# Kernel optimization log

Hardware: AMD Instinct MI355X
Metric: run time of the kernel (lower is better)

## Reference

```python
import jax, jax.numpy as jnp
import numpy as np

N = 8192
F_IN, F_HID, F_OUT = 256, 256, 64


def setup_inputs() -> dict:
    key = jax.random.key(0)
    k1, k2, k3, k4 = jax.random.split(key, 4)
    adj = jax.random.uniform(k1, (N, N), dtype=jnp.float32)
    x = jax.random.normal(k2, (N, F_IN), dtype=jnp.float32)
    W1 = jax.random.uniform(k3, (F_IN, F_HID), dtype=jnp.float32)
    W2 = jax.random.uniform(k4, (F_HID, F_OUT), dtype=jnp.float32)
    return {"adj": adj, "x": x, "W1": W1, "W2": W2}


def reference(adj, x, W1, W2):
    # Layer 1: left_to_right -> (adj @ x) @ W1, then ReLU (dropout is identity in eval)
    h = jnp.matmul(jnp.matmul(adj, x), W1)
    h = jax.nn.relu(h)
    # Layer 2 (last): no activation
    h = jnp.matmul(jnp.matmul(adj, h), W2)
    # Final log_softmax over class dim
    return jax.nn.log_softmax(h, axis=1)
```

## Files before the change

### kernel.cpp

```cpp
#include <hip/hip_runtime.h>

typedef short bf16x8 __attribute__((ext_vector_type(8)));
typedef float f32x4 __attribute__((ext_vector_type(4)));
typedef unsigned short us8 __attribute__((ext_vector_type(8)));

__device__ __forceinline__ unsigned short f2bf(float f) {
    unsigned int u = __float_as_uint(f);
    u += 0x7fffu + ((u >> 16) & 1u);
    return (unsigned short)(u >> 16);
}

__device__ __forceinline__ void hard_barrier() {
    asm volatile("s_waitcnt lgkmcnt(0)" ::: "memory");
    __builtin_amdgcn_sched_barrier(0);
    __builtin_amdgcn_s_barrier();
    __builtin_amdgcn_sched_barrier(0);
}

__global__ __launch_bounds__(256) void transpose_cast_kernel(
    const float* __restrict__ in, unsigned short* __restrict__ out, int R, int Cc) {
    __shared__ alignas(16) unsigned short sT[64][65];
    const int r0 = blockIdx.x * 64, c0 = blockIdx.y * 64;
    const int t = threadIdx.x;
#pragma unroll
    for (int p = 0; p < 16; ++p) {
        int flat = p * 256 + t;
        int r = flat >> 6, c = flat & 63;
        sT[c][r] = f2bf(in[(size_t)(r0 + r) * Cc + (c0 + c)]);
    }
    __syncthreads();
#pragma unroll
    for (int p = 0; p < 16; ++p) {
        int flat = p * 256 + t;
        int c = flat >> 6, r = flat & 63;
        out[(size_t)(c0 + c) * R + (r0 + r)] = sT[c][r];
    }
}

template<int BN, int WM, int WN, int AMODE, bool TOUT, typename OutT>
__global__ __launch_bounds__(256) void gemm_kernel(
    const void* __restrict__ Aptr, const unsigned short* __restrict__ BT,
    OutT* __restrict__ C, int M, int N, int K, long aslab) {
    constexpr int BM = 64, BK = 64, LDW = 72;
    constexpr int MF = BM / WM / 16;
    constexpr int NF = BN / WN / 16;
    __shared__ alignas(16) unsigned short sA[BM * LDW];
    __shared__ alignas(16) unsigned short sB[BN * LDW];
    const int t = threadIdx.x;
    const int w = t >> 6, l = t & 63;
    const int wr = w / WN, wc = w % WN;
    const int m0 = blockIdx.x * BM;

    f32x4 acc[MF][NF] = {};

    for (int k0 = 0; k0 < K; k0 += BK) {
        const float* A32 = (const float*)Aptr;
#pragma unroll
        for (int p = 0; p < 4; ++p) {
            int flat = p * 256 + t;
            int row = flat >> 4, c4 = flat & 15;
            size_t base = (size_t)(m0 + row) * K + k0 + c4 * 4;
            float4 v = *(const float4*)&A32[base];
            if constexpr (AMODE == 2) {
                float4 b = *(const float4*)&A32[aslab + base];
                float4 c = *(const float4*)&A32[2 * aslab + base];
                float4 d = *(const float4*)&A32[3 * aslab + base];
                v.x = fmaxf(v.x + b.x + c.x + d.x, 0.f);
                v.y = fmaxf(v.y + b.y + c.y + d.y, 0.f);
                v.z = fmaxf(v.z + b.z + c.z + d.z, 0.f);
                v.w = fmaxf(v.w + b.w + c.w + d.w, 0.f);
            }
            ushort4 o = make_ushort4(f2bf(v.x), f2bf(v.y), f2bf(v.z), f2bf(v.w));
            *(ushort4*)&sA[row * LDW + c4 * 4] = o;
        }
#pragma unroll
        for (int p = 0; p < BN * 8 / 256; ++p) {
            int flat = p * 256 + t;
            int row = flat >> 3, c8 = flat & 7;
            us8 v = *(const us8*)&BT[(size_t)row * K + k0 + c8 * 8];
            *(us8*)&sB[row * LDW + c8 * 8] = v;
        }
        __syncthreads();
#pragma unroll
        for (int kk = 0; kk < BK; kk += 32) {
            bf16x8 av[MF], bv[NF];
#pragma unroll
            for (int m = 0; m < MF; ++m)
                av[m] = *(const bf16x8*)&sA[(wr * (BM / WM) + m * 16 + (l & 15)) * LDW + kk + (l >> 4) * 8];
#pragma unroll
            for (int n = 0; n < NF; ++n)
                bv[n] = *(const bf16x8*)&sB[(wc * (BN / WN) + n * 16 + (l & 15)) * LDW + kk + (l >> 4) * 8];
#pragma unroll
            for (int m = 0; m < MF; ++m)
#pragma unroll
                for (int n = 0; n < NF; ++n)
                    acc[m][n] = __builtin_amdgcn_mfma_f32_16x16x32_bf16(av[m], bv[n], acc[m][n], 0, 0, 0);
        }
        __syncthreads();
    }

#pragma unroll
    for (int m = 0; m < MF; ++m) {
#pragma unroll
        for (int n = 0; n < NF; ++n) {
            const int col = wc * (BN / WN) + n * 16 + (l & 15);
            const int rb = m0 + wr * (BM / WM) + m * 16 + ((l >> 4) << 2);
            float v0 = acc[m][n][0], v1 = acc[m][n][1], v2 = acc[m][n][2], v3 = acc[m][n][3];
            if constexpr (TOUT) {
                ushort4 o = make_ushort4(f2bf(v0), f2bf(v1), f2bf(v2), f2bf(v3));
                *(ushort4*)((unsigned short*)C + (size_t)col * M + rb) = o;
            } else {
                C[(size_t)(rb + 0) * N + col] = (OutT)v0;
                C[(size_t)(rb + 1) * N + col] = (OutT)v1;
                C[(size_t)(rb + 2) * N + col] = (OutT)v2;
                C[(size_t)(rb + 3) * N + col] = (OutT)v3;
            }
        }
    }
}

template<int BM, int BN, int WM, int WN, int THREADS, int MINB>
__global__ __launch_bounds__(THREADS, MINB) void pipe_gemm_kernel(
    const float* __restrict__ A, const unsigned short* __restrict__ BT,
    float* __restrict__ C, int M, int N, int K) {
    constexpr int BK = 64, LDW = 72;
    constexpr int MF = BM / WM / 16, NF = BN / WN / 16;
    constexpr int ACH = BM * BK / 4 / THREADS;
    constexpr int BCH = BN * BK / 8 / THREADS;
    static_assert(ACH * THREADS * 4 == BM * BK && BCH * THREADS * 8 == BN * BK, "split");
    __shared__ alignas(16) unsigned short sA[2][BM * LDW];
    __shared__ alignas(16) unsigned short sB[2][BN * LDW];
    const int t = threadIdx.x, w = t >> 6, l = t & 63;
    const int wr = w / WN, wc = w % WN;
    const int nx = gridDim.x;
    const int lin = blockIdx.x + nx * blockIdx.z;
    const int cpx = (nx * gridDim.z) >> 3;
    const int sw = (lin & 7) * cpx + (lin >> 3);
    const int bx = sw % nx, bz = sw / nx;
    const int m0 = bx * BM;
    const int klen = K / gridDim.z, kbeg = bz * klen;
    const int NT = klen / BK;
    float* Cp = C + (size_t)bz * M * N;

    float4 a0[ACH], a1[ACH];
    us8 b0[BCH], b1[BCH];

    auto LOAD = [&](float4 (&ar)[ACH], us8 (&br)[BCH], int k0) {
#pragma unroll
        for (int p = 0; p < ACH; ++p) {
            int flat = p * THREADS + t, row = flat >> 4, c4 = flat & 15;
            ar[p] = *(const float4*)&A[(size_t)(m0 + row) * K + k0 + c4 * 4];
        }
#pragma unroll
        for (int p = 0; p < BCH; ++p) {
            int flat = p * THREADS + t, row = flat >> 3, c8 = flat & 7;
            br[p] = *(const us8*)&BT[(size_t)row * K + k0 + c8 * 8];
        }
    };
    auto WRITE = [&](float4 (&ar)[ACH], us8 (&br)[BCH], int buf) {
#pragma unroll
        for (int p = 0; p < ACH; ++p) {
            int flat = p * THREADS + t, row = flat >> 4, c4 = flat & 15;
            float4 v = ar[p];
            *(ushort4*)&sA[buf][row * LDW + c4 * 4] =
                make_ushort4(f2bf(v.x), f2bf(v.y), f2bf(v.z), f2bf(v.w));
        }
#pragma unroll
        for (int p = 0; p < BCH; ++p) {
            int flat = p * THREADS + t, row = flat >> 3, c8 = flat & 7;
            *(us8*)&sB[buf][row * LDW + c8 * 8] = br[p];
        }
    };

    f32x4 acc[MF][NF] = {};

    auto COMPUTE = [&](int buf) {
#pragma unroll
        for (int kk = 0; kk < BK; kk += 32) {
            bf16x8 av[MF], bv[NF];
#pragma unroll
            for (int m = 0; m < MF; ++m)
                av[m] = *(const bf16x8*)&sA[buf][(wr * (BM / WM) + m * 16 + (l & 15)) * LDW + kk + (l >> 4) * 8];
#pragma unroll
            for (int n = 0; n < NF; ++n)
                bv[n] = *(const bf16x8*)&sB[buf][(wc * (BN / WN) + n * 16 + (l & 15)) * LDW + kk + (l >> 4) * 8];
#pragma unroll
            for (int m = 0; m < MF; ++m)
#pragma unroll
                for (int n = 0; n < NF; ++n)
                    acc[m][n] = __builtin_amdgcn_mfma_f32_16x16x32_bf16(av[m], bv[n], acc[m][n], 0, 0, 0);
        }
    };

    LOAD(a0, b0, kbeg);
    LOAD(a1, b1, kbeg + BK);
    WRITE(a0, b0, 0);
    hard_barrier();

    for (int tt = 0; tt < NT; tt += 2) {
        if (tt + 2 < NT) LOAD(a0, b0, kbeg + (tt + 2) * BK);
        __builtin_amdgcn_sched_barrier(0);
        COMPUTE(0);
        if (tt + 1 < NT) WRITE(a1, b1, 1);
        hard_barrier();
        if (tt + 1 < NT) {
            if (tt + 3 < NT) LOAD(a1, b1, kbeg + (tt + 3) * BK);
            __builtin_amdgcn_sched_barrier(0);
            COMPUTE(1);
            if (tt + 2 < NT) WRITE(a0, b0, 0);
            hard_barrier();
        }
    }

#pragma unroll
    for (int m = 0; m < MF; ++m)
#pragma unroll
        for (int n = 0; n < NF; ++n) {
            const int col = wc * (BN / WN) + n * 16 + (l & 15);
            const int rb = m0 + wr * (BM / WM) + m * 16 + ((l >> 4) << 2);
#pragma unroll
            for (int j = 0; j < 4; ++j)
                Cp[(size_t)(rb + j) * N + col] = acc[m][n][j];
        }
}

__global__ __launch_bounds__(256) void head2_kernel(
    const float* __restrict__ p, float* __restrict__ out, int M) {
    const int t = threadIdx.x, w = t >> 6, l = t & 63;
    const size_t stride = (size_t)M * 64;
#pragma unroll
    for (int rr = 0; rr < 4; ++rr) {
        int i = blockIdx.x * 16 + w * 4 + rr;
        size_t off = (size_t)i * 64 + l;
        float v = 0.f;
#pragma unroll
        for (int s = 0; s < 8; ++s) v += p[s * stride + off];
        float mx = v;
#pragma unroll
        for (int o = 32; o; o >>= 1) mx = fmaxf(mx, __shfl_xor(mx, o));
        float d0 = v - mx;
        float e = __expf(d0);
#pragma unroll
        for (int o = 32; o; o >>= 1) e += __shfl_xor(e, o);
        out[off] = d0 - __logf(e);
    }
}

extern "C" void kernel_launch(void* const* d_in, const int* in_sizes, int n_in,
                              void* d_out, int out_size, void* d_ws, size_t ws_size,
                              hipStream_t stream) {
    const float* adj = (const float*)d_in[0];
    const float* x   = (const float*)d_in[1];
    const float* W1  = (const float*)d_in[2];
    const float* W2  = (const float*)d_in[3];
    float* out = (float*)d_out;

    const int M = 8192, K = 8192;
    char* ws = (char*)d_ws;
    float*          pbuf1 = (float*)ws;
    float*          pbuf2 = (float*)(ws + 33554432);
    unsigned short* zT    = (unsigned short*)(ws + 50331648);
    unsigned short* hwT   = (unsigned short*)(ws + 54525952);
    unsigned short* W1T   = (unsigned short*)(ws + 55574528);
    unsigned short* W2T   = (unsigned short*)(ws + 55705600);

    transpose_cast_kernel<<<dim3(4, 4), 256, 0, stream>>>(W1, W1T, 256, 256);
    transpose_cast_kernel<<<dim3(4, 1), 256, 0, stream>>>(W2, W2T, 256, 64);
    gemm_kernel<256, 1, 4, 1, true, unsigned short>
        <<<dim3(M / 64), 256, 0, stream>>>(x, W1T, zT, M, 256, 256, 0);
    pipe_gemm_kernel<128, 256, 4, 4, 1024, 1>
        <<<dim3(M / 128, 1, 4), 1024, 0, stream>>>(adj, zT, pbuf1, M, 256, K);
    gemm_kernel<64, 2, 2, 2, true, unsigned short>
        <<<dim3(M / 64), 256, 0, stream>>>(pbuf1, W2T, hwT, M, 64, 256, (long)M * 256);
    pipe_gemm_kernel<128, 64, 4, 2, 512, 2>
        <<<dim3(M / 128, 1, 8), 512, 0, stream>>>(adj, hwT, pbuf2, M, 64, K);
    head2_kernel<<<dim3(M / 16), 256, 0, stream>>>(pbuf2, out, M);
}
```

Baseline: 158.0 us.

## Write bf16 copy of adj in first pass and reuse it in second GEMM

The first adjacency GEMM now writes its bf16-converted A tiles out to a workspace buffer as a side effect. The second adjacency GEMM then reads that bf16 copy instead of the fp32 adj, halving its A-operand traffic. The extra 128MB write in the first pass costs bandwidth, so the net gain depends on the second pass being memory-bound. The MFMA inner loop is also reordered to load B fragments one at a time, which lowers register pressure.

New measurement: 179.4 us. 13.5% more time.

```diff
diff --git a/kernel.cpp b/kernel.cpp
--- a/kernel.cpp
+++ b/kernel.cpp
@@ -1,4 +1,5 @@
 #include <hip/hip_runtime.h>
+#include <type_traits>
 
 typedef short bf16x8 __attribute__((ext_vector_type(8)));
 typedef float f32x4 __attribute__((ext_vector_type(4)));
@@ -119,15 +120,15 @@
     }
 }
 
-template<int BM, int BN, int WM, int WN, int THREADS, int MINB>
+template<int BM, int BN, int WM, int WN, int THREADS, int MINB, bool ABF16, bool ASIDE>
 __global__ __launch_bounds__(THREADS, MINB) void pipe_gemm_kernel(
-    const float* __restrict__ A, const unsigned short* __restrict__ BT,
-    float* __restrict__ C, int M, int N, int K) {
+    const void* __restrict__ Aptr, const unsigned short* __restrict__ BT,
+    float* __restrict__ C, unsigned short* __restrict__ Aside, int M, int N, int K) {
     constexpr int BK = 64, LDW = 72;
     constexpr int MF = BM / WM / 16, NF = BN / WN / 16;
-    constexpr int ACH = BM * BK / 4 / THREADS;
+    constexpr int ACH = ABF16 ? (BM * BK / 8 / THREADS) : (BM * BK / 4 / THREADS);
     constexpr int BCH = BN * BK / 8 / THREADS;
-    static_assert(ACH * THREADS * 4 == BM * BK && BCH * THREADS * 8 == BN * BK, "split");
+    using AT = typename std::conditional<ABF16, us8, float4>::type;
     __shared__ alignas(16) unsigned short sA[2][BM * LDW];
     __shared__ alignas(16) unsigned short sB[2][BN * LDW];
     const int t = threadIdx.x, w = t >> 6, l = t & 63;
@@ -142,14 +143,20 @@
     const int NT = klen / BK;
     float* Cp = C + (size_t)bz * M * N;
 
-    float4 a0[ACH], a1[ACH];
+    AT a0[ACH], a1[ACH];
     us8 b0[BCH], b1[BCH];
 
-    auto LOAD = [&](float4 (&ar)[ACH], us8 (&br)[BCH], int k0) {
+    auto LOAD = [&](AT (&ar)[ACH], us8 (&br)[BCH], int k0) {
 #pragma unroll
         for (int p = 0; p < ACH; ++p) {
-            int flat = p * THREADS + t, row = flat >> 4, c4 = flat & 15;
-            ar[p] = *(const float4*)&A[(size_t)(m0 + row) * K + k0 + c4 * 4];
+            int flat = p * THREADS + t;
+            if constexpr (ABF16) {
+                int row = flat >> 3, c8 = flat & 7;
+                ar[p] = *(const us8*)&((const unsigned short*)Aptr)[(size_t)(m0 + row) * K + k0 + c8 * 8];
+            } else {
+                int row = flat >> 4, c4 = flat & 15;
+                ar[p] = *(const float4*)&((const float*)Aptr)[(size_t)(m0 + row) * K + k0 + c4 * 4];
+            }
         }
 #pragma unroll
         for (int p = 0; p < BCH; ++p) {
@@ -157,13 +164,21 @@
             br[p] = *(const us8*)&BT[(size_t)row * K + k0 + c8 * 8];
         }
     };
-    auto WRITE = [&](float4 (&ar)[ACH], us8 (&br)[BCH], int buf) {
+    auto WRITE = [&](AT (&ar)[ACH], us8 (&br)[BCH], int buf, int k0) {
 #pragma unroll
         for (int p = 0; p < ACH; ++p) {
-            int flat = p * THREADS + t, row = flat >> 4, c4 = flat & 15;
-            float4 v = ar[p];
-            *(ushort4*)&sA[buf][row * LDW + c4 * 4] =
-                make_ushort4(f2bf(v.x), f2bf(v.y), f2bf(v.z), f2bf(v.w));
+            int flat = p * THREADS + t;
+            if constexpr (ABF16) {
+                int row = flat >> 3, c8 = flat & 7;
+                *(us8*)&sA[buf][row * LDW + c8 * 8] = ar[p];
+            } else {
+                int row = flat >> 4, c4 = flat & 15;
+                float4 v = ar[p];
+                ushort4 o = make_ushort4(f2bf(v.x), f2bf(v.y), f2bf(v.z), f2bf(v.w));
+                *(ushort4*)&sA[buf][row * LDW + c4 * 4] = o;
+                if constexpr (ASIDE)
+                    *(ushort4*)&Aside[(size_t)(m0 + row) * K + k0 + c4 * 4] = o;
+            }
         }
 #pragma unroll
         for (int p = 0; p < BCH; ++p) {
@@ -177,37 +192,36 @@
     auto COMPUTE = [&](int buf) {
 #pragma unroll
         for (int kk = 0; kk < BK; kk += 32) {
-            bf16x8 av[MF], bv[NF];
+            bf16x8 av[MF];
 #pragma unroll
             for (int m = 0; m < MF; ++m)
                 av[m] = *(const bf16x8*)&sA[buf][(wr * (BM / WM) + m * 16 + (l & 15)) * LDW + kk + (l >> 4) * 8];
 #pragma unroll
-            for (int n = 0; n < NF; ++n)
-                bv[n] = *(const bf16x8*)&sB[buf][(wc * (BN / WN) + n * 16 + (l & 15)) * LDW + kk + (l >> 4) * 8];
-#pragma unroll
-            for (int m = 0; m < MF; ++m)
-#pragma unroll
-                for (int n = 0; n < NF; ++n)
-                    acc[m][n] = __builtin_amdgcn_mfma_f32_16x16x32_bf16(av[m], bv[n], acc[m][n], 0, 0, 0);
+            for (int n = 0; n < NF; ++n) {
+                bf16x8 bv = *(const bf16x8*)&sB[buf][(wc * (BN / WN) + n * 16 + (l & 15)) * LDW + kk + (l >> 4) * 8];
+#pragma unroll
+                for (int m = 0; m < MF; ++m)
+                    acc[m][n] = __builtin_amdgcn_mfma_f32_16x16x32_bf16(av[m], bv, acc[m][n], 0, 0, 0);
+            }
         }
     };
 
     LOAD(a0, b0, kbeg);
     LOAD(a1, b1, kbeg + BK);
-    WRITE(a0, b0, 0);
+    WRITE(a0, b0, 0, kbeg);
     hard_barrier();
 
     for (int tt = 0; tt < NT; tt += 2) {
         if (tt + 2 < NT) LOAD(a0, b0, kbeg + (tt + 2) * BK);
         __builtin_amdgcn_sched_barrier(0);
         COMPUTE(0);
-        if (tt + 1 < NT) WRITE(a1, b1, 1);
+        if (tt + 1 < NT) WRITE(a1, b1, 1, kbeg + (tt + 1) * BK);
         hard_barrier();
         if (tt + 1 < NT) {
             if (tt + 3 < NT) LOAD(a1, b1, kbeg + (tt + 3) * BK);
             __builtin_amdgcn_sched_barrier(0);
             COMPUTE(1);
-            if (tt + 2 < NT) WRITE(a0, b0, 0);
+            if (tt + 2 < NT) WRITE(a0, b0, 0, kbeg + (tt + 2) * BK);
             hard_barrier();
         }
     }
@@ -263,16 +277,17 @@
     unsigned short* hwT   = (unsigned short*)(ws + 54525952);
     unsigned short* W1T   = (unsigned short*)(ws + 55574528);
     unsigned short* W2T   = (unsigned short*)(ws + 55705600);
+    unsigned short* adj16 = (unsigned short*)(ws + 67108864);
 
     transpose_cast_kernel<<<dim3(4, 4), 256, 0, stream>>>(W1, W1T, 256, 256);
     transpose_cast_kernel<<<dim3(4, 1), 256, 0, stream>>>(W2, W2T, 256, 64);
     gemm_kernel<256, 1, 4, 1, true, unsigned short>
         <<<dim3(M / 64), 256, 0, stream>>>(x, W1T, zT, M, 256, 256, 0);
-    pipe_gemm_kernel<128, 256, 4, 4, 1024, 1>
-        <<<dim3(M / 128, 1, 4), 1024, 0, stream>>>(adj, zT, pbuf1, M, 256, K);
+    pipe_gemm_kernel<128, 256, 4, 4, 1024, 1, false, true>
+        <<<dim3(M / 128, 1, 4), 1024, 0, stream>>>(adj, zT, pbuf1, adj16, M, 256, K);
     gemm_kernel<64, 2, 2, 2, true, unsigned short>
         <<<dim3(M / 64), 256, 0, stream>>>(pbuf1, W2T, hwT, M, 64, 256, (long)M * 256);
-    pipe_gemm_kernel<128, 64, 4, 2, 512, 2>
-        <<<dim3(M / 128, 1, 8), 512, 0, stream>>>(adj, hwT, pbuf2, M, 64, K);
+    pipe_gemm_kernel<128, 64, 4, 2, 512, 2, true, false>
+        <<<dim3(M / 128, 1, 8), 512, 0, stream>>>(adj16, hwT, pbuf2, nullptr, M, 64, K);
     head2_kernel<<<dim3(M / 16), 256, 0, stream>>>(pbuf2, out, M);
 }
```
